# Kernel optimization log

Measured on AMD Instinct MI355X. Metric: run time of the kernel, lower is better.

## Reference

```python
import jax, jax.numpy as jnp
import numpy as np

NUM_HEADS = 16

def setup_inputs() -> dict:
    key = jax.random.key(0)
    ks = jax.random.split(key, 6)
    B, S, D = 2, 2048, 1024
    return {
        "hidden_states": jax.random.normal(ks[0], (B, S, D), dtype=jnp.float32),
        "c_attn_w": jax.random.normal(ks[1], (D, 3 * D), dtype=jnp.float32) * 0.02,
        "c_attn_b": jax.random.normal(ks[2], (3 * D,), dtype=jnp.float32) * 0.02,
        "attn_bias": jax.random.normal(ks[3], (S, S), dtype=jnp.float32) * 0.02,
        "c_proj_w": jax.random.normal(ks[4], (D, D), dtype=jnp.float32) * 0.02,
        "c_proj_b": jax.random.normal(ks[5], (D,), dtype=jnp.float32) * 0.02,
    }

def reference(hidden_states, c_attn_w, c_attn_b, attn_bias, c_proj_w, c_proj_b):
    B, S, D = hidden_states.shape
    H = NUM_HEADS
    hd = D // H
    # fused QKV projection: [B,S,3D]
    qkv = hidden_states @ c_attn_w + c_attn_b
    q, k, v = jnp.split(qkv, 3, axis=-1)
    # [B,H,S,hd]
    q = q.reshape(B, S, H, hd).transpose(0, 2, 1, 3)
    k = k.reshape(B, S, H, hd).transpose(0, 2, 1, 3)
    v = v.reshape(B, S, H, hd).transpose(0, 2, 1, 3)
    # scores [B,H,S,S] with learned additive bias and causal mask
    scores = jnp.einsum('bhqd,bhkd->bhqk', q, k) / jnp.sqrt(jnp.float32(hd))
    scores = scores + attn_bias[:S, :S][None, None, :, :]
    causal = jnp.tril(jnp.ones((S, S), dtype=bool))
    scores = jnp.where(causal[None, None, :, :], scores, jnp.float32(-1e9))
    attn = jax.nn.softmax(scores, axis=-1)
    ctx = jnp.einsum('bhqk,bhkd->bhqd', attn, v)
    ctx = ctx.transpose(0, 2, 1, 3).reshape(B, S, D)
    out = ctx @ c_proj_w + c_proj_b  # resid dropout is identity in eval
    return (out, k, v)
```

## Files before the change

### kernel.cpp

```cpp
#include <hip/hip_runtime.h>
#include <hip/hip_bf16.h>
#include <stdint.h>


typedef __attribute__((ext_vector_type(4))) float f32x4;
typedef __attribute__((ext_vector_type(16))) float f32x16;
typedef __attribute__((ext_vector_type(8))) short s16x8;
typedef __attribute__((ext_vector_type(4))) short s16x4;
typedef unsigned short u16;

#define LOG2E 1.4426950408889634f
#define QSCALE 0.18033688011112042f

__device__ __forceinline__ u16 f2bf(float f) {
  unsigned w;
  asm("v_cvt_pk_bf16_f32 %0, %1, %2" : "=v"(w) : "v"(f), "v"(f));
  return (u16)w;
}
__device__ __forceinline__ unsigned cvtpk(float lo, float hi) {
  unsigned w;
  asm("v_cvt_pk_bf16_f32 %0, %1, %2" : "=v"(w) : "v"(lo), "v"(hi));
  return w;
}
__device__ __forceinline__ float bf2f(u16 h) {
  unsigned int x = ((unsigned int)h) << 16;
  return __builtin_bit_cast(float, x);
}
__device__ __forceinline__ float fexp2(float x) {
  float r;
  asm("v_exp_f32 %0, %1" : "=v"(r) : "v"(x));
  return r;
}
__device__ __forceinline__ void pl32swap(unsigned& a, unsigned& b) {
  asm volatile("v_permlane32_swap_b32 %0, %1" : "+v"(a), "+v"(b));
}
__device__ __forceinline__ s16x8 frag8(unsigned a, unsigned b, unsigned c, unsigned d) {
  union { unsigned u[4]; s16x8 v; } t;
  t.u[0] = a; t.u[1] = b; t.u[2] = c; t.u[3] = d;
  return t.v;
}
__device__ __forceinline__ f32x16 mfma32(s16x8 a, s16x8 b, f32x16 c) {
  return __builtin_amdgcn_mfma_f32_32x32x16_bf16(a, b, c, 0, 0, 0);
}

__device__ __forceinline__ void gload_lds16(const u16* g, u16* lds) {
  __builtin_amdgcn_global_load_lds(
      (const __attribute__((address_space(1))) unsigned int*)g,
      (__attribute__((address_space(3))) unsigned int*)lds, 16, 0, 0);
}


__global__ __launch_bounds__(256) void prepass_fused(
    const float* __restrict__ hs, u16* __restrict__ hsb,
    const float* __restrict__ Wqkv, u16* __restrict__ wqkvT,
    const float* __restrict__ Wproj, u16* __restrict__ wprojT) {
  __shared__ float tile[32][33];
  const int id = blockIdx.x;
  if (id < 4096) {
    const int i = id * 256 + threadIdx.x;
    f32x4 v = *(const f32x4*)&hs[(size_t)i * 4];
    s16x4 o;
    o[0] = (short)f2bf(v[0]); o[1] = (short)f2bf(v[1]);
    o[2] = (short)f2bf(v[2]); o[3] = (short)f2bf(v[3]);
    *(s16x4*)&hsb[(size_t)i * 4] = o;
    return;
  }
  const bool qkv = (id < 7168);
  const int tw = qkv ? id - 4096 : id - 7168;
  const int nx = qkv ? 96 : 32;
  const float* W = qkv ? Wqkv : Wproj;
  u16* WT = qkv ? wqkvT : wprojT;
  const int N = qkv ? 3072 : 1024, K = 1024;
  const int n0 = (tw % nx) * 32, k0 = (tw / nx) * 32;
  const int tx = threadIdx.x & 31, ty = threadIdx.x >> 5;
#pragma unroll
  for (int i = 0; i < 32; i += 8)
    tile[ty + i][tx] = W[(size_t)(k0 + ty + i) * N + (n0 + tx)];
  __syncthreads();
#pragma unroll
  for (int i = 0; i < 32; i += 8)
    WT[(size_t)(n0 + ty + i) * K + (k0 + tx)] = f2bf(tile[tx][ty + i]);
}


__global__ __launch_bounds__(256) void bias_tile(const float* __restrict__ B,
                                                 u16* __restrict__ T) {
  const int cell = blockIdx.x * 2 + (threadIdx.x >> 7);
  const int kt = cell & 31, q32 = cell >> 5;
  if (kt > (q32 >> 1)) return;
  const int tid7 = threadIdx.x & 127;
  const int t = tid7 >> 6, lane = tid7 & 63;
  const int hh = q32 >> 1;
  const size_t boff = (size_t)(hh + (q32 & 1)) * (hh + 1);
  const int q = q32 * 32 + (lane & 31);
  const int kb = kt * 64 + t * 32 + 4 * (lane >> 5);
  u16 vv[16];
#pragma unroll
  for (int r = 0; r < 16; r++) {
    const int k = kb + (r & 3) + 8 * (r >> 2);
    vv[r] = (k <= q) ? f2bf(B[(size_t)q * 2048 + k] * LOG2E) : (u16)0xFF80;
  }
  u16* dst = T + (boff + kt) * 2048 + t * 1024 + (size_t)lane * 16;
  *(s16x8*)dst = *(s16x8*)&vv[0];
  *(s16x8*)(dst + 8) = *(s16x8*)&vv[8];
}


template <int MODE>
__global__ __launch_bounds__(256) void gemm_bt(
    const u16* __restrict__ A, const u16* __restrict__ BT,
    const float* __restrict__ bias, float* __restrict__ outF,
    u16* __restrict__ q_ws, u16* __restrict__ k_ws, u16* __restrict__ vT_ws,
    int M, int N, int K) {
  __shared__ u16 As[2][128 * 32];
  __shared__ u16 Bs[2][128 * 32];
  const int nwg = gridDim.x * gridDim.y;
  int flat = blockIdx.y * gridDim.x + blockIdx.x;
  flat = (flat & 7) * (nwg >> 3) + (flat >> 3);
  const int m0 = (flat / gridDim.x) * 128, n0 = (flat % gridDim.x) * 128;
  const int tid = threadIdx.x;
  const int wid = tid >> 6, lane = tid & 63;
  const int c = lane & 15, hi = lane >> 4;
  const int wm = wid >> 1, wn = wid & 1;
  const int srow = lane >> 2;
  const int skp = (lane & 3) * 8;

  f32x4 acc[4][4] = {};

#define STG(SLOT, K0)                                                         \
  {                                                                           \
    _Pragma("unroll")                                                         \
    for (int t = 0; t < 2; t++) {                                             \
      const int rowl = wid * 32 + t * 16;                                     \
      gload_lds16(&A[(size_t)(m0 + rowl + srow) * K + (K0) + skp],            \
                  &As[SLOT][rowl * 32]);                                      \
      gload_lds16(&BT[(size_t)(n0 + rowl + srow) * K + (K0) + skp],           \
                  &Bs[SLOT][rowl * 32]);                                      \
    }                                                                         \
  }

  STG(0, 0);
  __syncthreads();

  int bufi = 0;
  for (int k0 = 0; k0 < K; k0 += 32) {
    if (k0 + 32 < K) {
      if (bufi) { STG(0, k0 + 32); } else { STG(1, k0 + 32); }
    }
    s16x8 af[4], bfr[4];
#pragma unroll
    for (int i = 0; i < 4; i++)
      af[i] = *(const s16x8*)&As[bufi][(wm * 64 + i * 16 + c) * 32 + hi * 8];
#pragma unroll
    for (int i = 0; i < 4; i++)
      bfr[i] = *(const s16x8*)&Bs[bufi][(wn * 64 + i * 16 + c) * 32 + hi * 8];
    __builtin_amdgcn_s_setprio(1);
#pragma unroll
    for (int i = 0; i < 4; i++)
#pragma unroll
      for (int j = 0; j < 4; j++)
        acc[i][j] = __builtin_amdgcn_mfma_f32_16x16x32_bf16(af[i], bfr[j], acc[i][j], 0, 0, 0);
    __builtin_amdgcn_s_setprio(0);
    __syncthreads();
    bufi ^= 1;
  }
#undef STG

  if (MODE == 1) {
#pragma unroll
    for (int i = 0; i < 4; i++) {
#pragma unroll
      for (int j = 0; j < 4; j++) {
        const int col = n0 + wn * 64 + j * 16 + c;
        const int rb = m0 + wm * 64 + i * 16 + hi * 4;
        const float bv = bias[col];
#pragma unroll
        for (int u = 0; u < 4; u++)
          outF[(size_t)(rb + u) * N + col] = acc[i][j][u] + bv;
      }
    }
  } else {
    const int which = n0 >> 10;
#pragma unroll
    for (int i = 0; i < 4; i++) {
#pragma unroll
      for (int j = 0; j < 4; j++) {
        const int col = n0 + wn * 64 + j * 16 + c;
        const int rb = m0 + wm * 64 + i * 16 + hi * 4;
        const float bv = bias[col];
        const int h = (col >> 6) & 15, d = col & 63;
        if (which == 2) {
          const int b = rb >> 11, s0 = rb & 2047;
#pragma unroll
          for (int u = 0; u < 4; u++)
            outF[8388608u + (size_t)(b * 16 + h) * 131072u + (size_t)(s0 + u) * 64 + d] =
                acc[i][j][u] + bv;
          uint2 w;
          w.x = cvtpk(acc[i][j][0] + bv, acc[i][j][1] + bv);
          w.y = cvtpk(acc[i][j][2] + bv, acc[i][j][3] + bv);
          *(uint2*)&vT_ws[(size_t)(b * 16 + h) * 131072u + (size_t)d * 2048 + s0] = w;
        } else {
#pragma unroll
          for (int u = 0; u < 4; u++) {
            const int r = rb + u;
            const int b = r >> 11, s = r & 2047;
            const size_t idx = (size_t)(b * 16 + h) * 131072u + (size_t)s * 64 + d;
            const float v = acc[i][j][u] + bv;
            if (which == 0) {
              q_ws[idx] = f2bf(v * QSCALE);
            } else {
              outF[4194304u + idx] = v;
              k_ws[idx] = f2bf(v);
            }
          }
        }
      }
    }
  }
}


__global__ __launch_bounds__(256, 4) void attn_fused(
    const u16* __restrict__ q_ws, const u16* __restrict__ k_ws,
    const u16* __restrict__ vT_ws, const u16* __restrict__ biasT,
    u16* __restrict__ ctx) {
  __shared__ u16 Ks[2][64 * 64];
  __shared__ u16 Vs[2][64 * 64];

  const int id = blockIdx.x;
  const int bh = (id & 7) * 4 + ((id >> 3) & 3);
  const int qblk = 31 - (id >> 5);

  const int wid = threadIdx.x >> 6, lane = threadIdx.x & 63;
  const int pq = wid >> 1, par = wid & 1;
  const int l31 = lane & 31, hi5 = lane >> 5;
  const int qrow0 = qblk * 64 + pq * 32;

  const u16* qh = q_ws + (size_t)bh * 131072u;
  const u16* kh = k_ws + (size_t)bh * 131072u;
  const u16* vh = vT_ws + (size_t)bh * 131072u;

  s16x8 qf[4];
#pragma unroll
  for (int s = 0; s < 4; s++)
    qf[s] = *(const s16x8*)&qh[(size_t)(qrow0 + l31) * 64 + s * 16 + hi5 * 8];

  const int q32 = qblk * 2 + pq;
  const int hh = q32 >> 1;
  const size_t boff = (size_t)(hh + (q32 & 1)) * (hh + 1);
  const u16* bbase = biasT + boff * 2048 + (size_t)par * 1024 + (size_t)lane * 16;

  const int sl_r = lane >> 3, sl_c = lane & 7;

  f32x16 o0 = {}, o1 = {};
  float mrow = -1e30f, lpart = 0.f;

#define STAGE(BUF, N0)                                                        \
  {                                                                           \
    _Pragma("unroll")                                                         \
    for (int t = 0; t < 2; t++) {                                             \
      const int rb = wid * 16 + t * 8;                                        \
      const int r = rb + sl_r;                                                \
      gload_lds16(&kh[(size_t)((N0) + r) * 64 + ((sl_c ^ (r & 7)) * 8)],      \
                  &Ks[BUF][rb * 64]);                                         \
      gload_lds16(&vh[(size_t)r * 2048 + (N0) + ((sl_c ^ (r & 7)) * 8)],      \
                  &Vs[BUF][rb * 64]);                                         \
    }                                                                         \
  }

  STAGE(0, 0);
  __syncthreads();

  int buf = 0;
  const int nkt = qblk + 1;
  const int swz = l31 & 7;
  const int arow = par * 32 + l31;

  s16x8 bc0 = *(const s16x8*)(bbase);
  s16x8 bc1 = *(const s16x8*)(bbase + 8);

  for (int kt = 0; kt < nkt; ++kt) {
    if (kt + 1 < nkt) {
      if (buf) { STAGE(0, kt * 64 + 64); } else { STAGE(1, kt * 64 + 64); }
    }
    const u16* btn = bbase + (size_t)((kt + 1 < nkt) ? kt + 1 : kt) * 2048;
    const s16x8 bn0 = *(const s16x8*)(btn);
    const s16x8 bn1 = *(const s16x8*)(btn + 8);

    f32x16 s0;
#pragma unroll
    for (int r = 0; r < 8; r++) {
      s0[r] = bf2f((u16)bc0[r]);
      s0[r + 8] = bf2f((u16)bc1[r]);
    }

    const u16* ksb = &Ks[buf][0];
    __builtin_amdgcn_s_setprio(1);
#pragma unroll
    for (int s = 0; s < 4; s++) {
      const int chq = ((s * 2 + hi5) ^ swz) * 8;
      const s16x8 a0 = *(const s16x8*)&ksb[arow * 64 + chq];
      s0 = mfma32(a0, qf[s], s0);
    }
    __builtin_amdgcn_s_setprio(0);

    float t0 = fmaxf(fmaxf(s0[0], s0[1]), fmaxf(s0[2], s0[3]));
    float t1 = fmaxf(fmaxf(s0[4], s0[5]), fmaxf(s0[6], s0[7]));
    float t2 = fmaxf(fmaxf(s0[8], s0[9]), fmaxf(s0[10], s0[11]));
    float t3 = fmaxf(fmaxf(s0[12], s0[13]), fmaxf(s0[14], s0[15]));
    float tm = fmaxf(fmaxf(t0, t1), fmaxf(t2, t3));
    tm = fmaxf(tm, __shfl_xor(tm, 32));

    if (__any(tm > mrow + 8.f)) {
      const float nm = fmaxf(mrow, tm);
      const float al = fexp2(mrow - nm);
      mrow = nm;
      lpart *= al;
#pragma unroll
      for (int r = 0; r < 16; r++) { o0[r] *= al; o1[r] *= al; }
    }

    float a0s = 0.f, a1s = 0.f;
#pragma unroll
    for (int r = 0; r < 8; r++) {
      s0[r] = fexp2(s0[r] - mrow);       a0s += s0[r];
      s0[r + 8] = fexp2(s0[r + 8] - mrow); a1s += s0[r + 8];
    }
    lpart += a0s + a1s;

    unsigned wv0 = cvtpk(s0[0], s0[1]),   wv1 = cvtpk(s0[2], s0[3]);
    unsigned wv2 = cvtpk(s0[4], s0[5]),   wv3 = cvtpk(s0[6], s0[7]);
    unsigned wv4 = cvtpk(s0[8], s0[9]),   wv5 = cvtpk(s0[10], s0[11]);
    unsigned wv6 = cvtpk(s0[12], s0[13]), wv7 = cvtpk(s0[14], s0[15]);
    pl32swap(wv0, wv2); pl32swap(wv1, wv3);
    pl32swap(wv4, wv6); pl32swap(wv5, wv7);

    const u16* vsb = &Vs[buf][0];
    __builtin_amdgcn_s_setprio(1);
#pragma unroll
    for (int hf = 0; hf < 2; hf++) {
      const s16x8 pa = hf ? frag8(wv4, wv5, wv6, wv7) : frag8(wv0, wv1, wv2, wv3);
      const int s = par * 2 + hf;
      const int chv = ((s * 2 + hi5) ^ swz) * 8;
      const s16x8 v0 = *(const s16x8*)&vsb[l31 * 64 + chv];
      const s16x8 v1 = *(const s16x8*)&vsb[(32 + l31) * 64 + chv];
      o0 = mfma32(pa, v0, o0);
      o1 = mfma32(pa, v1, o1);
    }
    __builtin_amdgcn_s_setprio(0);

    __syncthreads();
    buf ^= 1;
    bc0 = bn0; bc1 = bn1;
  }
#undef STAGE

  lpart += __shfl_xor(lpart, 32);

  float* obuf = (float*)&Ks[0][0];
  float2* mlb = (float2*)&Vs[0][0];

  __syncthreads();
  if (hi5 == 0) mlb[(par * 2 + pq) * 64 + l31] = make_float2(mrow, lpart);
  if (par == 1) {
    const int slot = pq * 64 + lane;
#pragma unroll
    for (int r = 0; r < 16; r++) {
      obuf[r * 128 + slot] = o0[r];
      obuf[(16 + r) * 128 + slot] = o1[r];
    }
  }
  __syncthreads();
  if (par == 0) {
    const int slot = pq * 64 + lane;
    const int b = bh >> 4, h = bh & 15;
#pragma unroll
    for (int r = 0; r < 16; r++) {
      const int qloc = (r & 3) + 8 * (r >> 2) + 4 * hi5;
      const float2 Aml = mlb[pq * 64 + qloc];
      const float2 Bml = mlb[(2 + pq) * 64 + qloc];
      const float mm = fmaxf(Aml.x, Bml.x);
      const float fa = fexp2(Aml.x - mm), fb = fexp2(Bml.x - mm);
      const float inv = __builtin_amdgcn_rcpf(Aml.y * fa + Bml.y * fb);
      const float om0 = (o0[r] * fa + obuf[r * 128 + slot] * fb) * inv;
      const float om1 = (o1[r] * fa + obuf[(16 + r) * 128 + slot] * fb) * inv;
      const int tok = b * 2048 + qrow0 + qloc;
      ctx[(size_t)tok * 1024 + h * 64 + l31] = f2bf(om0);
      ctx[(size_t)tok * 1024 + h * 64 + 32 + l31] = f2bf(om1);
    }
  }
}


extern "C" void kernel_launch(void* const* d_in, const int* in_sizes, int n_in,
                              void* d_out, int out_size, void* d_ws, size_t ws_size,
                              hipStream_t stream) {
  const float* hs        = (const float*)d_in[0];
  const float* c_attn_w  = (const float*)d_in[1];
  const float* c_attn_b  = (const float*)d_in[2];
  const float* attn_bias = (const float*)d_in[3];
  const float* c_proj_w  = (const float*)d_in[4];
  const float* c_proj_b  = (const float*)d_in[5];
  float* out = (float*)d_out;

  uint8_t* ws = (uint8_t*)d_ws;
  u16* hsb    = (u16*)(ws + 0);
  u16* wqkvT  = (u16*)(ws + 8388608u);
  u16* wprojT = (u16*)(ws + 14680064u);
  u16* q_ws   = (u16*)(ws + 16777216u);
  u16* k_ws   = (u16*)(ws + 25165824u);
  u16* vT_ws  = (u16*)(ws + 33554432u);
  u16* ctx    = (u16*)(ws + 41943040u);
  u16* biasT  = hsb;

  prepass_fused<<<8192, 256, 0, stream>>>(hs, hsb, c_attn_w, wqkvT, c_proj_w, wprojT);

  gemm_bt<0><<<dim3(24, 32), 256, 0, stream>>>(hsb, wqkvT, c_attn_b, out,
                                               q_ws, k_ws, vT_ws, 4096, 3072, 1024);

  bias_tile<<<1024, 256, 0, stream>>>(attn_bias, biasT);

  attn_fused<<<dim3(1024), 256, 0, stream>>>(q_ws, k_ws, vT_ws, biasT, ctx);

  gemm_bt<1><<<dim3(8, 32), 256, 0, stream>>>(ctx, wprojT, c_proj_b, out,
                                              (u16*)nullptr, (u16*)nullptr, (u16*)nullptr,
                                              4096, 1024, 1024);
}
```

Baseline: 121.3 us.

## Fuse bias tiling into prepass and stage V-transpose stores through LDS

The attention-bias tiling kernel is folded into the prepass launch as extra blocks, with its output moved into the not-yet-written region of the output buffer so it no longer aliases the bf16 hidden-state buffer. The separate As/Bs shared arrays in the GEMM are merged into one buffer. In the QKV epilogue, V-transposed tiles are written into that buffer with an XOR swizzle and then stored to global memory as coalesced 16-byte rows, replacing scattered 8-byte stores. The aim is to save one kernel launch and make the vT writes coalesced, at the cost of an extra LDS round trip and a barrier in the epilogue.

```diff
diff --git a/kernel.cpp b/kernel.cpp
--- a/kernel.cpp
+++ b/kernel.cpp
@@ -53,7 +53,8 @@
 __global__ __launch_bounds__(256) void prepass_fused(
     const float* __restrict__ hs, u16* __restrict__ hsb,
     const float* __restrict__ Wqkv, u16* __restrict__ wqkvT,
-    const float* __restrict__ Wproj, u16* __restrict__ wprojT) {
+    const float* __restrict__ Wproj, u16* __restrict__ wprojT,
+    const float* __restrict__ B, u16* __restrict__ biasT) {
   __shared__ float tile[32][33];
   const int id = blockIdx.x;
   if (id < 4096) {
@@ -65,27 +66,25 @@
     *(s16x4*)&hsb[(size_t)i * 4] = o;
     return;
   }
-  const bool qkv = (id < 7168);
-  const int tw = qkv ? id - 4096 : id - 7168;
-  const int nx = qkv ? 96 : 32;
-  const float* W = qkv ? Wqkv : Wproj;
-  u16* WT = qkv ? wqkvT : wprojT;
-  const int N = qkv ? 3072 : 1024, K = 1024;
-  const int n0 = (tw % nx) * 32, k0 = (tw / nx) * 32;
-  const int tx = threadIdx.x & 31, ty = threadIdx.x >> 5;
-#pragma unroll
-  for (int i = 0; i < 32; i += 8)
-    tile[ty + i][tx] = W[(size_t)(k0 + ty + i) * N + (n0 + tx)];
-  __syncthreads();
-#pragma unroll
-  for (int i = 0; i < 32; i += 8)
-    WT[(size_t)(n0 + ty + i) * K + (k0 + tx)] = f2bf(tile[tx][ty + i]);
-}
-
-
-__global__ __launch_bounds__(256) void bias_tile(const float* __restrict__ B,
-                                                 u16* __restrict__ T) {
-  const int cell = blockIdx.x * 2 + (threadIdx.x >> 7);
+  if (id < 8192) {
+    const bool qkv = (id < 7168);
+    const int tw = qkv ? id - 4096 : id - 7168;
+    const int nx = qkv ? 96 : 32;
+    const float* W = qkv ? Wqkv : Wproj;
+    u16* WT = qkv ? wqkvT : wprojT;
+    const int N = qkv ? 3072 : 1024, K = 1024;
+    const int n0 = (tw % nx) * 32, k0 = (tw / nx) * 32;
+    const int tx = threadIdx.x & 31, ty = threadIdx.x >> 5;
+#pragma unroll
+    for (int i = 0; i < 32; i += 8)
+      tile[ty + i][tx] = W[(size_t)(k0 + ty + i) * N + (n0 + tx)];
+    __syncthreads();
+#pragma unroll
+    for (int i = 0; i < 32; i += 8)
+      WT[(size_t)(n0 + ty + i) * K + (k0 + tx)] = f2bf(tile[tx][ty + i]);
+    return;
+  }
+  const int cell = (id - 8192) * 2 + (threadIdx.x >> 7);
   const int kt = cell & 31, q32 = cell >> 5;
   if (kt > (q32 >> 1)) return;
   const int tid7 = threadIdx.x & 127;
@@ -100,7 +99,7 @@
     const int k = kb + (r & 3) + 8 * (r >> 2);
     vv[r] = (k <= q) ? f2bf(B[(size_t)q * 2048 + k] * LOG2E) : (u16)0xFF80;
   }
-  u16* dst = T + (boff + kt) * 2048 + t * 1024 + (size_t)lane * 16;
+  u16* dst = biasT + (boff + kt) * 2048 + t * 1024 + (size_t)lane * 16;
   *(s16x8*)dst = *(s16x8*)&vv[0];
   *(s16x8*)(dst + 8) = *(s16x8*)&vv[8];
 }
@@ -112,8 +111,7 @@
     const float* __restrict__ bias, float* __restrict__ outF,
     u16* __restrict__ q_ws, u16* __restrict__ k_ws, u16* __restrict__ vT_ws,
     int M, int N, int K) {
-  __shared__ u16 As[2][128 * 32];
-  __shared__ u16 Bs[2][128 * 32];
+  __shared__ u16 SH[16384];
   const int nwg = gridDim.x * gridDim.y;
   int flat = blockIdx.y * gridDim.x + blockIdx.x;
   flat = (flat & 7) * (nwg >> 3) + (flat >> 3);
@@ -133,9 +131,9 @@
     for (int t = 0; t < 2; t++) {                                             \
       const int rowl = wid * 32 + t * 16;                                     \
       gload_lds16(&A[(size_t)(m0 + rowl + srow) * K + (K0) + skp],            \
-                  &As[SLOT][rowl * 32]);                                      \
+                  &SH[(SLOT) * 4096 + rowl * 32]);                            \
       gload_lds16(&BT[(size_t)(n0 + rowl + srow) * K + (K0) + skp],           \
-                  &Bs[SLOT][rowl * 32]);                                      \
+                  &SH[8192 + (SLOT) * 4096 + rowl * 32]);                     \
     }                                                                         \
   }
 
@@ -150,10 +148,10 @@
     s16x8 af[4], bfr[4];
 #pragma unroll
     for (int i = 0; i < 4; i++)
-      af[i] = *(const s16x8*)&As[bufi][(wm * 64 + i * 16 + c) * 32 + hi * 8];
+      af[i] = *(const s16x8*)&SH[bufi * 4096 + (wm * 64 + i * 16 + c) * 32 + hi * 8];
 #pragma unroll
     for (int i = 0; i < 4; i++)
-      bfr[i] = *(const s16x8*)&Bs[bufi][(wn * 64 + i * 16 + c) * 32 + hi * 8];
+      bfr[i] = *(const s16x8*)&SH[8192 + bufi * 4096 + (wn * 64 + i * 16 + c) * 32 + hi * 8];
     __builtin_amdgcn_s_setprio(1);
 #pragma unroll
     for (int i = 0; i < 4; i++)
@@ -181,25 +179,47 @@
     }
   } else {
     const int which = n0 >> 10;
-#pragma unroll
-    for (int i = 0; i < 4; i++) {
-#pragma unroll
-      for (int j = 0; j < 4; j++) {
-        const int col = n0 + wn * 64 + j * 16 + c;
-        const int rb = m0 + wm * 64 + i * 16 + hi * 4;
-        const float bv = bias[col];
-        const int h = (col >> 6) & 15, d = col & 63;
-        if (which == 2) {
-          const int b = rb >> 11, s0 = rb & 2047;
+    if (which == 2) {
+      const int b = m0 >> 11;
+      const int sg0 = m0 & 2047;
+#pragma unroll
+      for (int i = 0; i < 4; i++) {
+#pragma unroll
+        for (int j = 0; j < 4; j++) {
+          const int cc = wn * 64 + j * 16 + c;
+          const int col = n0 + cc;
+          const float bv = bias[col];
+          const int h = (col >> 6) & 15, d = col & 63;
+          const int sl = wm * 64 + i * 16 + hi * 4;
 #pragma unroll
           for (int u = 0; u < 4; u++)
-            outF[8388608u + (size_t)(b * 16 + h) * 131072u + (size_t)(s0 + u) * 64 + d] =
-                acc[i][j][u] + bv;
+            outF[8388608u + (size_t)(b * 16 + h) * 131072u +
+                 (size_t)(sg0 + sl + u) * 64 + d] = acc[i][j][u] + bv;
           uint2 w;
           w.x = cvtpk(acc[i][j][0] + bv, acc[i][j][1] + bv);
           w.y = cvtpk(acc[i][j][2] + bv, acc[i][j][3] + bv);
-          *(uint2*)&vT_ws[(size_t)(b * 16 + h) * 131072u + (size_t)d * 2048 + s0] = w;
-        } else {
+          *(uint2*)&SH[cc * 128 + (sl ^ ((cc & 7) << 3))] = w;
+        }
+      }
+      __syncthreads();
+#pragma unroll
+      for (int p = 0; p < 8; p++) {
+        const int cc = (tid >> 4) + p * 16;
+        const int sl0 = (tid & 15) * 8;
+        const s16x8 v8 = *(const s16x8*)&SH[cc * 128 + (sl0 ^ ((cc & 7) << 3))];
+        const int col = n0 + cc;
+        const int h = (col >> 6) & 15, d = col & 63;
+        *(s16x8*)&vT_ws[(size_t)(b * 16 + h) * 131072u + (size_t)d * 2048 + sg0 + sl0] = v8;
+      }
+    } else {
+#pragma unroll
+      for (int i = 0; i < 4; i++) {
+#pragma unroll
+        for (int j = 0; j < 4; j++) {
+          const int col = n0 + wn * 64 + j * 16 + c;
+          const int rb = m0 + wm * 64 + i * 16 + hi * 4;
+          const float bv = bias[col];
+          const int h = (col >> 6) & 15, d = col & 63;
 #pragma unroll
           for (int u = 0; u < 4; u++) {
             const int r = rb + u;
@@ -411,14 +431,13 @@
   u16* k_ws   = (u16*)(ws + 25165824u);
   u16* vT_ws  = (u16*)(ws + 33554432u);
   u16* ctx    = (u16*)(ws + 41943040u);
-  u16* biasT  = hsb;
-
-  prepass_fused<<<8192, 256, 0, stream>>>(hs, hsb, c_attn_w, wqkvT, c_proj_w, wprojT);
+  u16* biasT  = (u16*)out;
+
+  prepass_fused<<<9216, 256, 0, stream>>>(hs, hsb, c_attn_w, wqkvT,
+                                          c_proj_w, wprojT, attn_bias, biasT);
 
   gemm_bt<0><<<dim3(24, 32), 256, 0, stream>>>(hsb, wqkvT, c_attn_b, out,
                                                q_ws, k_ws, vT_ws, 4096, 3072, 1024);
-
-  bias_tile<<<1024, 256, 0, stream>>>(attn_bias, biasT);
 
   attn_fused<<<dim3(1024), 256, 0, stream>>>(q_ws, k_ws, vT_ws, biasT, ctx);
 
```

New measurement: 131.4 us. +8.4%, slower.
